# Kernel optimization log

Hardware: AMD Instinct MI355X
Metric: run time of the kernel (lower is better)

## Reference

```python
import jax, jax.numpy as jnp
import numpy as np

N_NODES = 100000
N_EDGES = 3200000


def gcn_conv(x, src, dst, W, b, n):
    # PyG GCNConv: add self-loops, symmetric normalization, scatter-add to dst.
    loops = jnp.arange(n)
    s = jnp.concatenate([src, loops])
    d = jnp.concatenate([dst, loops])
    h = x @ W                                   # [N, out]
    deg = jnp.zeros((n,), h.dtype).at[d].add(1.0)
    dinv = jnp.where(deg > 0, jax.lax.rsqrt(deg), 0.0)
    norm = dinv[s] * dinv[d]                    # [E+N]
    msg = h[s] * norm[:, None]                  # gather + scale
    out = jax.ops.segment_sum(msg, d, num_segments=n)
    return out + b


def setup_inputs() -> dict:
    key = jax.random.key(0)
    ks = jax.random.split(key, 10)
    x1 = jax.random.normal(ks[0], (N_NODES, 3), dtype=jnp.float32)
    edge_index1 = jax.random.randint(ks[1], (2, N_EDGES), 0, N_NODES, dtype=jnp.int64 if jax.config.jax_enable_x64 else jnp.int32)
    def lin(k, fi, fo):
        s = 1.0 / np.sqrt(fi)
        kw, kb = jax.random.split(k)
        return (jax.random.uniform(kw, (fi, fo), jnp.float32, -s, s),
                jax.random.uniform(kb, (fo,), jnp.float32, -s, s))
    W11, b11 = lin(ks[2], 3, 32)
    W12, b12 = lin(ks[3], 32, 32)
    W13, b13 = lin(ks[4], 32, 32)
    fc_w, fc_b = lin(ks[5], 32, 1)
    return {"x1": x1, "edge_index1": edge_index1,
            "W11": W11, "b11": b11, "W12": W12, "b12": b12,
            "W13": W13, "b13": b13, "fc_w": fc_w, "fc_b": fc_b}


def reference(x1, edge_index1, W11, b11, W12, b12, W13, b13, fc_w, fc_b):
    n = x1.shape[0]
    src, dst = edge_index1[0], edge_index1[1]
    h = gcn_conv(x1, src, dst, W11, b11, n)
    h = jax.nn.relu(h)
    h = gcn_conv(h, src, dst, W12, b12, n)
    h = jax.nn.relu(h)
    h = gcn_conv(h, src, dst, W13, b13, n)
    h = jax.nn.relu(h)
    return h @ fc_w + fc_b                      # [N, 1]
```

## Files before the change

kernel.cpp:

```cpp
#include <hip/hip_runtime.h>
#include <hip/hip_bf16.h>
#include <hip/hip_fp16.h>


#define RBITS  7
#define RNODES 128
#define SBITS  12
#define SNODES 4096
#define BPS    32
#define SMAX   32
#define CE     4096
#define EPT    16

__global__ void k_init(int S, int B, int capS, int capB,
                       int* __restrict__ gcur1, int* __restrict__ gcur2) {
    int t = blockIdx.x * blockDim.x + threadIdx.x;
    if (t < S) gcur1[t] = t * capS;
    if (t < B) gcur2[t] = t * capB;
}

__global__ void k_bin1(const int* __restrict__ src, const int* __restrict__ dst, int E, int S,
                       int* __restrict__ gcur1, unsigned* __restrict__ binned1) {
    __shared__ int cnt[SMAX * 8];
    __shared__ int repOff[SMAX * 8];
    __shared__ int runS[SMAX];
    int tid = threadIdx.x, rep = tid & 7;
    for (int i = tid; i < SMAX * 8; i += 256) cnt[i] = 0;
    __syncthreads();
    int e0 = blockIdx.x * CE;
    int pk[EPT], rnk[EPT], sup[EPT];
#pragma unroll
    for (int j = 0; j < EPT; j++) {
        int e = e0 + j * 256 + tid;
        if (e < E) {
            int d = __builtin_nontemporal_load(dst + e);
            sup[j] = d >> SBITS;
            pk[j]  = (__builtin_nontemporal_load(src + e) << SBITS) | (d & (SNODES - 1));
            rnk[j] = atomicAdd(&cnt[sup[j] * 8 + rep], 1);
        } else sup[j] = -1;
    }
    __syncthreads();
    if (tid < S) {
        int tot = 0;
#pragma unroll
        for (int r = 0; r < 8; r++) { repOff[tid * 8 + r] = tot; tot += cnt[tid * 8 + r]; }
        runS[tid] = tot ? atomicAdd(&gcur1[tid], tot) : 0;
    }
    __syncthreads();
#pragma unroll
    for (int j = 0; j < EPT; j++)
        if (sup[j] >= 0)
            binned1[runS[sup[j]] + repOff[sup[j] * 8 + rep] + rnk[j]] = (unsigned)pk[j];
}

__global__ void k_bin2(const unsigned* __restrict__ binned1, const int* __restrict__ fillEnd,
                       int S, int capS, int* __restrict__ gcur2, unsigned* __restrict__ binned2) {
    __shared__ int send[SMAX];
    __shared__ int cnt[64 * 4];
    __shared__ int repOff[64 * 4];
    __shared__ int runS[64];
    int tid = threadIdx.x, rep = tid & 3;
    if (tid < S) send[tid] = fillEnd[tid];
    for (int i = tid; i < 64 * 4; i += 256) cnt[i] = 0;
    __syncthreads();
    int i0 = blockIdx.x * CE;
    int s0 = i0 / capS;
    int Sc = S * capS;
    unsigned pk[EPT];
    int rnk[EPT], rb[EPT];
#pragma unroll
    for (int j = 0; j < EPT; j++) {
        int idx = i0 + j * 256 + tid;
        rb[j] = -1;
        if (idx < Sc) {
            int sp = idx / capS;
            if (idx < send[sp]) {
                unsigned p = __builtin_nontemporal_load(binned1 + idx);
                int relB = ((sp - s0) << 5) | ((p >> RBITS) & (BPS - 1));
                pk[j] = p; rb[j] = relB;
                rnk[j] = atomicAdd(&cnt[relB * 4 + rep], 1);
            }
        }
    }
    __syncthreads();
    if (tid < 64) {
        int tot = 0;
#pragma unroll
        for (int r = 0; r < 4; r++) { repOff[tid * 4 + r] = tot; tot += cnt[tid * 4 + r]; }
        int sp = s0 + (tid >> 5);
        if (tot && sp < S) {
            int gb = sp * BPS + (tid & (BPS - 1));
            runS[tid] = atomicAdd(&gcur2[gb], tot);
        }
    }
    __syncthreads();
#pragma unroll
    for (int j = 0; j < EPT; j++)
        if (rb[j] >= 0) {
            unsigned p = pk[j];
            binned2[runS[rb[j]] + repOff[rb[j] * 4 + rep] + rnk[j]] =
                ((p >> SBITS) << RBITS) | (p & (RNODES - 1));
        }
}

__global__ void k_sortb2(const unsigned* __restrict__ binned2, const int* __restrict__ gcur2,
                         int capB, int N, int* __restrict__ ssort,
                         int2* __restrict__ row2, float* __restrict__ dinv) {
    __shared__ int cnt[RNODES];
    __shared__ int loc[RNODES];
    int b = blockIdx.x, tid = threadIdx.x;
    int beg = b * capB, end = gcur2[b];
    if (tid < RNODES) cnt[tid] = 0;
    __syncthreads();
    for (int idx = beg + tid; idx < end; idx += 256)
        atomicAdd(&cnt[__builtin_nontemporal_load(binned2 + idx) & (RNODES - 1)], 1);
    __syncthreads();
    if (tid < RNODES) loc[tid] = cnt[tid];
    __syncthreads();
    for (int off = 1; off < RNODES; off <<= 1) {
        int v = 0;
        if (tid < RNODES && tid >= off) v = loc[tid - off];
        __syncthreads();
        if (tid < RNODES) loc[tid] += v;
        __syncthreads();
    }
    int n0 = b << RBITS;
    if (tid < RNODES) {
        int excl = loc[tid] - cnt[tid];
        loc[tid] = beg + excl;
        int n = n0 + tid;
        if (n < N) {
            row2[n] = make_int2(beg + excl, beg + excl + cnt[tid]);
            dinv[n] = rsqrtf((float)cnt[tid] + 1.0f);
        }
    }
    if (tid < RNODES) cnt[tid] = 0;
    __syncthreads();
    for (int idx = beg + tid; idx < end; idx += 256) {
        unsigned p = __builtin_nontemporal_load(binned2 + idx);
        int dl = (int)(p & (RNODES - 1));
        int r  = atomicAdd(&cnt[dl], 1);
        ssort[loc[dl] + r] = (int)(p >> RBITS);
    }
}

__global__ void k_prep1(const float* __restrict__ x, const float* __restrict__ dinv,
                        float4* __restrict__ p4, int N) {
    int n = blockIdx.x * blockDim.x + threadIdx.x;
    if (n >= N) return;
    float di = dinv[n];
    p4[n] = make_float4(x[n * 3] * di, x[n * 3 + 1] * di, x[n * 3 + 2] * di, 0.f);
}

__global__ void k_l1g(const int2* __restrict__ row2, const int* __restrict__ ssort,
                      const float4* __restrict__ p4, const float* __restrict__ dinv,
                      const float* __restrict__ W1, const float* __restrict__ b1,
                      const float* __restrict__ W2, __half* __restrict__ g2, int N) {
    __shared__ float sW1[96];
    __shared__ float sb1[32];
    __shared__ float sW2[1024];
    __shared__ float sh1[256];
    int tid = threadIdx.x;
    for (int i = tid; i < 1024; i += 256) sW2[i] = W2[i];
    if (tid < 96) sW1[tid] = W1[tid];
    if (tid < 32) sb1[tid] = b1[tid];
    __syncthreads();
    int t = blockIdx.x * 256 + tid;
    int n = t >> 5, c = t & 31;
    bool active = (n < N);
    float ax = 0.f, ay = 0.f, az = 0.f;
    float di = 0.f;
    if (active) {
        int2 r = row2[n];
        for (int idx = r.x + c; idx < r.y; idx += 32) {
            float4 q = p4[__builtin_nontemporal_load(ssort + idx)];
            ax += q.x; ay += q.y; az += q.z;
        }
    }
#pragma unroll
    for (int off = 16; off; off >>= 1) {
        ax += __shfl_xor(ax, off, 32);
        ay += __shfl_xor(ay, off, 32);
        az += __shfl_xor(az, off, 32);
    }
    float h1 = 0.f;
    if (active) {
        float4 me = p4[n];
        di = dinv[n];
        ax = di * (ax + me.x); ay = di * (ay + me.y); az = di * (az + me.z);
        h1 = fmaxf(ax * sW1[c] + ay * sW1[32 + c] + az * sW1[64 + c] + sb1[c], 0.f);
    }
    sh1[tid] = h1;
    __syncthreads();
    if (!active) return;
    const float* hr = sh1 + (tid >> 5) * 32;
    float acc = 0.f;
#pragma unroll
    for (int k = 0; k < 32; k++) acc += hr[k] * sW2[k * 32 + c];
    g2[(size_t)n * 32 + c] = __float2half_rn(acc * di);
}

__global__ void k_agg16(const int2* __restrict__ row2, const int* __restrict__ ssort,
                        const __half2* __restrict__ g2, const float* __restrict__ dinv,
                        const float* __restrict__ bias, float* __restrict__ h, int N) {
    int t = blockIdx.x * blockDim.x + threadIdx.x;
    int n = t >> 4, l = t & 15;
    if (n >= N) return;
    int2 r = row2[n];
    int beg = r.x, end = r.y;
    float ax = 0.f, ay = 0.f, bx = 0.f, by = 0.f;
    float cx = 0.f, cy = 0.f, dx = 0.f, dy = 0.f;
    for (int base = beg; base < end; base += 16) {
        int m = end - base; if (m > 16) m = 16;
        int myS = (l < m) ? __builtin_nontemporal_load(ssort + base + l) : 0;
        int i = 0;
        for (; i + 4 <= m; i += 4) {
            int s0 = __shfl(myS, i,     16);
            int s1 = __shfl(myS, i + 1, 16);
            int s2 = __shfl(myS, i + 2, 16);
            int s3 = __shfl(myS, i + 3, 16);
            float2 q0 = __half22float2(g2[(size_t)s0 * 16 + l]);
            float2 q1 = __half22float2(g2[(size_t)s1 * 16 + l]);
            float2 q2 = __half22float2(g2[(size_t)s2 * 16 + l]);
            float2 q3 = __half22float2(g2[(size_t)s3 * 16 + l]);
            ax += q0.x; ay += q0.y;
            bx += q1.x; by += q1.y;
            cx += q2.x; cy += q2.y;
            dx += q3.x; dy += q3.y;
        }
        for (; i < m; i++) {
            int s = __shfl(myS, i, 16);
            float2 q = __half22float2(g2[(size_t)s * 16 + l]);
            ax += q.x; ay += q.y;
        }
    }
    float2 self = __half22float2(g2[(size_t)n * 16 + l]);
    float sx = ((ax + bx) + (cx + dx)) + self.x;
    float sy = ((ay + by) + (cy + dy)) + self.y;
    float di = dinv[n];
    int c0 = l * 2;
    float2 o = make_float2(fmaxf(di * sx + bias[c0], 0.f),
                           fmaxf(di * sy + bias[c0 + 1], 0.f));
    *(float2*)(h + (size_t)n * 32 + c0) = o;
}

__global__ void k_gemv32h(const float* __restrict__ h, const float* __restrict__ W,
                          const float* __restrict__ dinv, __half* __restrict__ g, int N) {
    __shared__ float sW[1024];
    __shared__ float sh[256];
    int tid = threadIdx.x;
    for (int i = tid; i < 1024; i += 256) sW[i] = W[i];
    int t = blockIdx.x * 256 + tid;
    if (t < N * 32) sh[tid] = h[t];
    __syncthreads();
    int n = t >> 5, c = t & 31;
    if (n >= N) return;
    const float* hr = sh + (tid >> 5) * 32;
    float acc = 0.f;
#pragma unroll
    for (int k = 0; k < 32; k++) acc += hr[k] * sW[k * 32 + c];
    g[t] = __float2half_rn(acc * dinv[n]);
}

__global__ void k_agg16_fc(const int2* __restrict__ row2, const int* __restrict__ ssort,
                           const __half2* __restrict__ g2, const float* __restrict__ dinv,
                           const float* __restrict__ bias, const float* __restrict__ fcw,
                           const float* __restrict__ fcb, float* __restrict__ out, int N) {
    int t = blockIdx.x * blockDim.x + threadIdx.x;
    int n = t >> 4, l = t & 15;
    if (n >= N) return;
    int2 r = row2[n];
    int beg = r.x, end = r.y;
    float ax = 0.f, ay = 0.f, bx = 0.f, by = 0.f;
    float cx = 0.f, cy = 0.f, dx = 0.f, dy = 0.f;
    for (int base = beg; base < end; base += 16) {
        int m = end - base; if (m > 16) m = 16;
        int myS = (l < m) ? __builtin_nontemporal_load(ssort + base + l) : 0;
        int i = 0;
        for (; i + 4 <= m; i += 4) {
            int s0 = __shfl(myS, i,     16);
            int s1 = __shfl(myS, i + 1, 16);
            int s2 = __shfl(myS, i + 2, 16);
            int s3 = __shfl(myS, i + 3, 16);
            float2 q0 = __half22float2(g2[(size_t)s0 * 16 + l]);
            float2 q1 = __half22float2(g2[(size_t)s1 * 16 + l]);
            float2 q2 = __half22float2(g2[(size_t)s2 * 16 + l]);
            float2 q3 = __half22float2(g2[(size_t)s3 * 16 + l]);
            ax += q0.x; ay += q0.y;
            bx += q1.x; by += q1.y;
            cx += q2.x; cy += q2.y;
            dx += q3.x; dy += q3.y;
        }
        for (; i < m; i++) {
            int s = __shfl(myS, i, 16);
            float2 q = __half22float2(g2[(size_t)s * 16 + l]);
            ax += q.x; ay += q.y;
        }
    }
    float2 self = __half22float2(g2[(size_t)n * 16 + l]);
    float sx = ((ax + bx) + (cx + dx)) + self.x;
    float sy = ((ay + by) + (cy + dy)) + self.y;
    float di = dinv[n];
    int c0 = l * 2;
    float v = fmaxf(di * sx + bias[c0], 0.f) * fcw[c0]
            + fmaxf(di * sy + bias[c0 + 1], 0.f) * fcw[c0 + 1];
    v += __shfl_down(v, 8, 16);
    v += __shfl_down(v, 4, 16);
    v += __shfl_down(v, 2, 16);
    v += __shfl_down(v, 1, 16);
    if (l == 0) out[n] = v + fcb[0];
}

extern "C" void kernel_launch(void* const* d_in, const int* in_sizes, int n_in,
                              void* d_out, int out_size, void* d_ws, size_t ws_size,
                              hipStream_t stream) {
    const float* x1  = (const float*)d_in[0];
    const int*   ei  = (const int*)d_in[1];
    const float* W11 = (const float*)d_in[2];
    const float* b11 = (const float*)d_in[3];
    const float* W12 = (const float*)d_in[4];
    const float* b12 = (const float*)d_in[5];
    const float* W13 = (const float*)d_in[6];
    const float* b13 = (const float*)d_in[7];
    const float* fcw = (const float*)d_in[8];
    const float* fcb = (const float*)d_in[9];
    float* out = (float*)d_out;

    const int N = in_sizes[0] / 3;
    const int E = in_sizes[1] / 2;
    const int* src = ei;
    const int* dst = ei + E;

    const int B = (N + RNODES - 1) / RNODES;
    const int S = (N + SNODES - 1) / SNODES;
    const int capS = E / S + E / S / 16 + 1024;
    const int capB = E / B + E / B / 4 + 256;
    const size_t NC = (size_t)N * 32;

    float4*   p4      = (float4*)d_ws;
    __half*   g       = (__half*)(p4 + N);
    int2*     row2    = (int2*)(g + NC);
    float*    dinv    = (float*)(row2 + N);
    int*      gcur1   = (int*)(dinv + N);
    int*      gcur2   = gcur1 + 32;
    unsigned* binned1 = (unsigned*)(gcur2 + 800);
    unsigned* binned2 = binned1 + (size_t)S * capS;
    int*      ssort   = (int*)(binned2 + (size_t)B * capB);
    float*    h       = (float*)binned1;

    dim3 blk(256);
    dim3 grid_nc(((int)NC + 255) / 256);
    dim3 grid_n((N + 255) / 256);
    dim3 grid_n16(((N * 16) + 255) / 256);
    dim3 grid_e((E + CE - 1) / CE);
    dim3 grid_sc((S * capS + CE - 1) / CE);
    dim3 grid_b(B);

    k_init<<<dim3((B + 255) / 256), blk, 0, stream>>>(S, B, capS, capB, gcur1, gcur2);
    k_bin1<<<grid_e, blk, 0, stream>>>(src, dst, E, S, gcur1, binned1);
    k_bin2<<<grid_sc, blk, 0, stream>>>(binned1, gcur1, S, capS, gcur2, binned2);
    k_sortb2<<<grid_b, blk, 0, stream>>>(binned2, gcur2, capB, N, ssort, row2, dinv);

    k_prep1<<<grid_n, blk, 0, stream>>>(x1, dinv, p4, N);
    k_l1g<<<grid_nc, blk, 0, stream>>>(row2, ssort, p4, dinv, W11, b11, W12, g, N);

    k_agg16<<<grid_n16, blk, 0, stream>>>(row2, ssort, (const __half2*)g, dinv, b12, h, N);
    k_gemv32h<<<grid_nc, blk, 0, stream>>>(h, W13, dinv, g, N);

    k_agg16_fc<<<grid_n16, blk, 0, stream>>>(row2, ssort, (const __half2*)g, dinv, b13, fcw, fcb, out, N);
}
```

Before: 233.4 us.

## Split half-precision features into two column planes and aggregate each in separate passes

```diff
diff --git a/kernel.cpp b/kernel.cpp
--- a/kernel.cpp
+++ b/kernel.cpp
@@ -197,51 +197,53 @@
     float acc = 0.f;
 #pragma unroll
     for (int k = 0; k < 32; k++) acc += hr[k] * sW2[k * 32 + c];
-    g2[(size_t)n * 32 + c] = __float2half_rn(acc * di);
-}
-
-__global__ void k_agg16(const int2* __restrict__ row2, const int* __restrict__ ssort,
-                        const __half2* __restrict__ g2, const float* __restrict__ dinv,
-                        const float* __restrict__ bias, float* __restrict__ h, int N) {
+    size_t NP = (size_t)N * 16;
+    g2[(size_t)(c >> 4) * NP + (size_t)n * 16 + (c & 15)] = __float2half_rn(acc * di);
+}
+
+__global__ void k_agg8p(const int2* __restrict__ row2, const int* __restrict__ ssort,
+                        const __half2* __restrict__ gp, const float* __restrict__ dinv,
+                        const float* __restrict__ bias, float* __restrict__ hp, int N) {
     int t = blockIdx.x * blockDim.x + threadIdx.x;
-    int n = t >> 4, l = t & 15;
+    int n = t >> 3, l = t & 7;
     if (n >= N) return;
     int2 r = row2[n];
     int beg = r.x, end = r.y;
     float ax = 0.f, ay = 0.f, bx = 0.f, by = 0.f;
     float cx = 0.f, cy = 0.f, dx = 0.f, dy = 0.f;
-    for (int base = beg; base < end; base += 16) {
-        int m = end - base; if (m > 16) m = 16;
+    for (int base = beg; base < end; base += 8) {
+        int m = end - base; if (m > 8) m = 8;
         int myS = (l < m) ? __builtin_nontemporal_load(ssort + base + l) : 0;
         int i = 0;
         for (; i + 4 <= m; i += 4) {
-            int s0 = __shfl(myS, i,     16);
-            int s1 = __shfl(myS, i + 1, 16);
-            int s2 = __shfl(myS, i + 2, 16);
-            int s3 = __shfl(myS, i + 3, 16);
-            float2 q0 = __half22float2(g2[(size_t)s0 * 16 + l]);
-            float2 q1 = __half22float2(g2[(size_t)s1 * 16 + l]);
-            float2 q2 = __half22float2(g2[(size_t)s2 * 16 + l]);
-            float2 q3 = __half22float2(g2[(size_t)s3 * 16 + l]);
+            int s0 = __shfl(myS, i,     8);
+            int s1 = __shfl(myS, i + 1, 8);
+            int s2 = __shfl(myS, i + 2, 8);
+            int s3 = __shfl(myS, i + 3, 8);
+            float2 q0 = __half22float2(gp[(size_t)s0 * 8 + l]);
+            float2 q1 = __half22float2(gp[(size_t)s1 * 8 + l]);
+            float2 q2 = __half22float2(gp[(size_t)s2 * 8 + l]);
+            float2 q3 = __half22float2(gp[(size_t)s3 * 8 + l]);
             ax += q0.x; ay += q0.y;
             bx += q1.x; by += q1.y;
             cx += q2.x; cy += q2.y;
             dx += q3.x; dy += q3.y;
         }
         for (; i < m; i++) {
-            int s = __shfl(myS, i, 16);
-            float2 q = __half22float2(g2[(size_t)s * 16 + l]);
+            int s = __shfl(myS, i, 8);
+            float2 q = __half22float2(gp[(size_t)s * 8 + l]);
             ax += q.x; ay += q.y;
         }
     }
-    float2 self = __half22float2(g2[(size_t)n * 16 + l]);
+    float2 self = __half22float2(gp[(size_t)n * 8 + l]);
     float sx = ((ax + bx) + (cx + dx)) + self.x;
     float sy = ((ay + by) + (cy + dy)) + self.y;
     float di = dinv[n];
     int c0 = l * 2;
     float2 o = make_float2(fmaxf(di * sx + bias[c0], 0.f),
                            fmaxf(di * sy + bias[c0 + 1], 0.f));
-    *(float2*)(h + (size_t)n * 32 + c0) = o;
+    double od; __builtin_memcpy(&od, &o, 8);
+    __builtin_nontemporal_store(od, (double*)(hp + (size_t)n * 32 + c0));
 }
 
 __global__ void k_gemv32h(const float* __restrict__ h, const float* __restrict__ W,
@@ -259,56 +261,63 @@
     float acc = 0.f;
 #pragma unroll
     for (int k = 0; k < 32; k++) acc += hr[k] * sW[k * 32 + c];
-    g[t] = __float2half_rn(acc * dinv[n]);
-}
-
-__global__ void k_agg16_fc(const int2* __restrict__ row2, const int* __restrict__ ssort,
-                           const __half2* __restrict__ g2, const float* __restrict__ dinv,
-                           const float* __restrict__ bias, const float* __restrict__ fcw,
-                           const float* __restrict__ fcb, float* __restrict__ out, int N) {
+    size_t NP = (size_t)N * 16;
+    g[(size_t)(c >> 4) * NP + (size_t)n * 16 + (c & 15)] = __float2half_rn(acc * dinv[n]);
+}
+
+__global__ void k_aggfc8(const int2* __restrict__ row2, const int* __restrict__ ssort,
+                         const __half2* __restrict__ gp, const float* __restrict__ dinv,
+                         const float* __restrict__ bias, const float* __restrict__ fcw,
+                         const float* __restrict__ fcb, float* __restrict__ partial,
+                         float* __restrict__ out, int N, int pass) {
     int t = blockIdx.x * blockDim.x + threadIdx.x;
-    int n = t >> 4, l = t & 15;
+    int n = t >> 3, l = t & 7;
     if (n >= N) return;
     int2 r = row2[n];
     int beg = r.x, end = r.y;
     float ax = 0.f, ay = 0.f, bx = 0.f, by = 0.f;
     float cx = 0.f, cy = 0.f, dx = 0.f, dy = 0.f;
-    for (int base = beg; base < end; base += 16) {
-        int m = end - base; if (m > 16) m = 16;
+    for (int base = beg; base < end; base += 8) {
+        int m = end - base; if (m > 8) m = 8;
         int myS = (l < m) ? __builtin_nontemporal_load(ssort + base + l) : 0;
         int i = 0;
         for (; i + 4 <= m; i += 4) {
-            int s0 = __shfl(myS, i,     16);
-            int s1 = __shfl(myS, i + 1, 16);
-            int s2 = __shfl(myS, i + 2, 16);
-            int s3 = __shfl(myS, i + 3, 16);
-            float2 q0 = __half22float2(g2[(size_t)s0 * 16 + l]);
-            float2 q1 = __half22float2(g2[(size_t)s1 * 16 + l]);
-            float2 q2 = __half22float2(g2[(size_t)s2 * 16 + l]);
-            float2 q3 = __half22float2(g2[(size_t)s3 * 16 + l]);
+            int s0 = __shfl(myS, i,     8);
+            int s1 = __shfl(myS, i + 1, 8);
+            int s2 = __shfl(myS, i + 2, 8);
+            int s3 = __shfl(myS, i + 3, 8);
+            float2 q0 = __half22float2(gp[(size_t)s0 * 8 + l]);
+            float2 q1 = __half22float2(gp[(size_t)s1 * 8 + l]);
+            float2 q2 = __half22float2(gp[(size_t)s2 * 8 + l]);
+            float2 q3 = __half22float2(gp[(size_t)s3 * 8 + l]);
             ax += q0.x; ay += q0.y;
             bx += q1.x; by += q1.y;
             cx += q2.x; cy += q2.y;
             dx += q3.x; dy += q3.y;
         }
         for (; i < m; i++) {
-            int s = __shfl(myS, i, 16);
-            float2 q = __half22float2(g2[(size_t)s * 16 + l]);
+            int s = __shfl(myS, i, 8);
+            float2 q = __half22float2(gp[(size_t)s * 8 + l]);
             ax += q.x; ay += q.y;
         }
     }
-    float2 self = __half22float2(g2[(size_t)n * 16 + l]);
+    float2 self = __half22float2(gp[(size_t)n * 8 + l]);
     float sx = ((ax + bx) + (cx + dx)) + self.x;
     float sy = ((ay + by) + (cy + dy)) + self.y;
     float di = dinv[n];
     int c0 = l * 2;
     float v = fmaxf(di * sx + bias[c0], 0.f) * fcw[c0]
             + fmaxf(di * sy + bias[c0 + 1], 0.f) * fcw[c0 + 1];
-    v += __shfl_down(v, 8, 16);
-    v += __shfl_down(v, 4, 16);
-    v += __shfl_down(v, 2, 16);
-    v += __shfl_down(v, 1, 16);
-    if (l == 0) out[n] = v + fcb[0];
+    v += __shfl_down(v, 4, 8);
+    v += __shfl_down(v, 2, 8);
+    v += __shfl_down(v, 1, 8);
+    if (l == 0) {
+        if (pass == 0) {
+            __builtin_nontemporal_store(v, partial + n);
+        } else {
+            out[n] = v + __builtin_nontemporal_load(partial + n) + fcb[0];
+        }
+    }
 }
 
 extern "C" void kernel_launch(void* const* d_in, const int* in_sizes, int n_in,
@@ -347,11 +356,15 @@
     unsigned* binned2 = binned1 + (size_t)S * capS;
     int*      ssort   = (int*)(binned2 + (size_t)B * capB);
     float*    h       = (float*)binned1;
+    float*    partial = (float*)binned2;
+
+    __half* gA = g;
+    __half* gB = g + (size_t)N * 16;
 
     dim3 blk(256);
     dim3 grid_nc(((int)NC + 255) / 256);
     dim3 grid_n((N + 255) / 256);
-    dim3 grid_n16(((N * 16) + 255) / 256);
+    dim3 grid_n8(((N * 8) + 255) / 256);
     dim3 grid_e((E + CE - 1) / CE);
     dim3 grid_sc((S * capS + CE - 1) / CE);
     dim3 grid_b(B);
@@ -364,8 +377,10 @@
     k_prep1<<<grid_n, blk, 0, stream>>>(x1, dinv, p4, N);
     k_l1g<<<grid_nc, blk, 0, stream>>>(row2, ssort, p4, dinv, W11, b11, W12, g, N);
 
-    k_agg16<<<grid_n16, blk, 0, stream>>>(row2, ssort, (const __half2*)g, dinv, b12, h, N);
+    k_agg8p<<<grid_n8, blk, 0, stream>>>(row2, ssort, (const __half2*)gA, dinv, b12, h, N);
+    k_agg8p<<<grid_n8, blk, 0, stream>>>(row2, ssort, (const __half2*)gB, dinv, b12 + 16, h + 16, N);
     k_gemv32h<<<grid_nc, blk, 0, stream>>>(h, W13, dinv, g, N);
 
-    k_agg16_fc<<<grid_n16, blk, 0, stream>>>(row2, ssort, (const __half2*)g, dinv, b13, fcw, fcb, out, N);
-}
+    k_aggfc8<<<grid_n8, blk, 0, stream>>>(row2, ssort, (const __half2*)gA, dinv, b13, fcw, nullptr, partial, nullptr, N, 0);
+    k_aggfc8<<<grid_n8, blk, 0, stream>>>(row2, ssort, (const __half2*)gB, dinv, b13 + 16, fcw + 16, fcb, partial, out, N, 1);
+}
```

Result: slower. 295.7 us (+26.7%).
